# Optimization experiments

Hardware: AMD Instinct MI355X
Metric: run time of the kernel (lower is better)

Reference implementation:

```python
import jax, jax.numpy as jnp
import numpy as np

SIGMA = 0.5          # kernel length_scale
SOFTNESS = 1.0       # softmax temperature scaling
B, F, J, M, U = 4096, 512, 16, 64, 512  # batch, feature, num_domains, domain_dim, units


def _gauss(sqdist):
    # ExponentiatedQuadratic with amplitude=1: exp(-||x-y||^2 / (2*sigma^2))
    return jnp.exp(-sqdist / (2.0 * SIGMA * SIGMA))


def setup_inputs() -> dict:
    key = jax.random.key(0)
    k1, k2, k3 = jax.random.split(key, 3)
    h = jax.random.normal(k1, (B, F), dtype=jnp.float32)
    # domain basis: keras RandomNormal() default stddev=0.05
    domains = 0.05 * jax.random.normal(k2, (J, M, F), dtype=jnp.float32)
    # W_domains: GlorotUniform over (M, U)
    limit = np.sqrt(6.0 / (M + U)).astype(np.float32)
    W = jax.random.uniform(k3, (J, M, U), dtype=jnp.float32, minval=-limit, maxval=limit)
    b = jnp.zeros((J, U), dtype=jnp.float32)
    return {"h": h, "domains": domains, "W": W, "b": b}


def reference(h, domains, W, b):
    # ---- kernel matrix between inputs and all domain bases: K[b,j,m] ----
    h2 = jnp.sum(h * h, axis=-1)                      # [B]
    d2 = jnp.sum(domains * domains, axis=-1)          # [J,M]
    cross = jnp.einsum('bf,jmf->bjm', h, domains)     # [B,J,M]
    K_hd = _gauss(h2[:, None, None] + d2[None] - 2.0 * cross)

    # ---- per-domain MMD: k(x,x) - 2*mean_m k(x,d_m) + mean_{m,m'} k(d_m,d_m') ----
    dd = d2[:, :, None] + d2[:, None, :] - 2.0 * jnp.einsum('jmf,jnf->jmn', domains, domains)
    k_dd_mean = jnp.mean(_gauss(dd), axis=(1, 2))     # [J]
    mmd = 1.0 - 2.0 * jnp.mean(K_hd, axis=2) + k_dd_mean[None, :]  # [B,J]

    # softmax over domains of -softness * mmd  -> domain probabilities [B,J]
    prob = jax.nn.softmax(-SOFTNESS * mmd, axis=1)

    # ---- representer outputs per domain: K(h, D_j) @ W_j + b_j ----
    out = jnp.einsum('bjm,jmu->bju', K_hd, W) + b[None]  # [B,J,U]

    # probability-weighted sum over domains
    return jnp.einsum('bj,bju->bu', prob, out)           # [B,U]
```

## Files before the change

### kernel.cpp

```cpp
#include <hip/hip_runtime.h>
#include <math.h>

typedef unsigned short ushort_t;
typedef __attribute__((ext_vector_type(8))) short bf16x8;
typedef __attribute__((ext_vector_type(4))) float f32x4;

#define B_SZ 4096
#define F_SZ 512
#define J_SZ 16
#define M_SZ 64
#define U_SZ 512
#define P_SZ 1024

__device__ __forceinline__ ushort_t f2bf(float f) {
    union { float f; unsigned int u; } v; v.f = f;
    unsigned int r = (v.u + 0x7FFFu + ((v.u >> 16) & 1u)) >> 16;
    return (ushort_t)r;
}

__device__ __forceinline__ void gload_lds16(const void* g, void* l) {
    __builtin_amdgcn_global_load_lds(
        (const __attribute__((address_space(1))) unsigned int*)g,
        (__attribute__((address_space(3))) unsigned int*)l, 16, 0, 0);
}

__global__ __launch_bounds__(256) void prep_kernel(const float* __restrict__ h,
                                                   const float* __restrict__ dom,
                                                   const float* __restrict__ W,
                                                   ushort_t* __restrict__ hbf,
                                                   ushort_t* __restrict__ dombf,
                                                   ushort_t* __restrict__ Wt,
                                                   float* __restrict__ h2,
                                                   float* __restrict__ d2,
                                                   float* __restrict__ Gpart) {
    const int bid = blockIdx.x;
    const int tid = threadIdx.x;

    if (bid < 1024) {
        int b = bid * 4 + (tid >> 6);
        int lane = tid & 63;
        const float4* row = (const float4*)(h + (size_t)b * F_SZ);
        ushort4* orow = (ushort4*)(hbf + (size_t)b * F_SZ);
        float s = 0.f;
        for (int i = lane; i < F_SZ / 4; i += 64) {
            float4 v = row[i];
            s += v.x * v.x + v.y * v.y + v.z * v.z + v.w * v.w;
            ushort4 o; o.x = f2bf(v.x); o.y = f2bf(v.y); o.z = f2bf(v.z); o.w = f2bf(v.w);
            orow[i] = o;
        }
        for (int off = 32; off; off >>= 1) s += __shfl_down(s, off);
        if (lane == 0) h2[b] = s;
    } else if (bid < 1280) {
        int p = (bid - 1024) * 4 + (tid >> 6);
        int lane = tid & 63;
        const float4* row = (const float4*)(dom + (size_t)p * F_SZ);
        ushort4* orow = (ushort4*)(dombf + (size_t)p * F_SZ);
        float s = 0.f;
        for (int i = lane; i < F_SZ / 4; i += 64) {
            float4 v = row[i];
            s += v.x * v.x + v.y * v.y + v.z * v.z + v.w * v.w;
            ushort4 o; o.x = f2bf(v.x); o.y = f2bf(v.y); o.z = f2bf(v.z); o.w = f2bf(v.w);
            orow[i] = o;
        }
        for (int off = 32; off; off >>= 1) s += __shfl_down(s, off);
        if (lane == 0) d2[p] = s;
    } else if (bid < 1344) {
        int idx = bid - 1280;
        int j = idx >> 2, kc = idx & 3;
        const float* base = dom + (size_t)j * M_SZ * F_SZ + kc * 128;
        __shared__ float As[32][68];
        int tx = tid & 15, ty = tid >> 4;
        float c[4][4] = {};
        for (int kk = 0; kk < 128; kk += 32) {
            for (int l = 0; l < 2; ++l) {
                int s = tid + l * 256;
                int r = s >> 3, c4 = (s & 7) << 2;
                float4 v = *(const float4*)&base[(size_t)r * F_SZ + kk + c4];
                As[c4 + 0][r] = v.x; As[c4 + 1][r] = v.y;
                As[c4 + 2][r] = v.z; As[c4 + 3][r] = v.w;
            }
            __syncthreads();
            for (int k = 0; k < 32; ++k) {
                float a[4], bv[4];
                for (int i = 0; i < 4; ++i) a[i] = As[k][ty * 4 + i];
                for (int i = 0; i < 4; ++i) bv[i] = As[k][tx * 4 + i];
                for (int i = 0; i < 4; ++i)
                    for (int l2 = 0; l2 < 4; ++l2) c[i][l2] += a[i] * bv[l2];
            }
            __syncthreads();
        }
        float* gout = Gpart + ((size_t)kc * 16 + j) * 4096;
        for (int i = 0; i < 4; ++i)
            for (int l2 = 0; l2 < 4; ++l2)
                gout[(ty * 4 + i) * 64 + tx * 4 + l2] = c[i][l2];
    } else {
        int idx = bid - 1344;
        int pt = (idx >> 3) * 64, ut = (idx & 7) * 64;
        __shared__ ushort_t T[64][72];
        for (int l = 0; l < 4; ++l) {
            int s = l * 256 + tid;
            int r = s >> 4, c4 = (s & 15) << 2;
            float4 v = *(const float4*)&W[(size_t)(pt + r) * U_SZ + ut + c4];
            T[c4 + 0][r] = f2bf(v.x); T[c4 + 1][r] = f2bf(v.y);
            T[c4 + 2][r] = f2bf(v.z); T[c4 + 3][r] = f2bf(v.w);
        }
        __syncthreads();
        for (int l = 0; l < 4; ++l) {
            int s = l * 256 + tid;
            int r2 = s >> 4, c4 = (s & 15) << 2;
            ushort4 o; o.x = T[r2][c4 + 0]; o.y = T[r2][c4 + 1];
            o.z = T[r2][c4 + 2]; o.w = T[r2][c4 + 3];
            *(ushort4*)&Wt[(size_t)(ut + r2) * P_SZ + pt + c4] = o;
        }
    }
}

__global__ __launch_bounds__(256) void gemm1_mfma(const ushort_t* __restrict__ hbf,
                                                  const ushort_t* __restrict__ dombf,
                                                  const float* __restrict__ h2,
                                                  const float* __restrict__ d2,
                                                  const float* __restrict__ Gpart,
                                                  ushort_t* __restrict__ Kbf,
                                                  float* __restrict__ sj,
                                                  float* __restrict__ kdd) {
    __shared__ ushort_t smem[24576];
    short* As = (short*)smem;
    short* Bs = (short*)(smem + 8192);
    const int b0 = blockIdx.x * 64;
    const int p0 = blockIdx.y * 128;
    const int tid = threadIdx.x;
    const int wid = tid >> 6, lane = tid & 63;
    const int wm = wid >> 1, wn = wid & 1;
    const int lcol = lane & 15, quad = lane >> 4;

    f32x4 acc[2][4];
    for (int i = 0; i < 2; ++i)
        for (int n = 0; n < 4; ++n) acc[i][n] = (f32x4){0.f, 0.f, 0.f, 0.f};

    for (int kk = 0; kk < F_SZ; kk += 128) {
#pragma unroll
        for (int l = 0; l < 4; ++l) {
            int s = l * 256 + tid;
            int row = s >> 4, c = s & 15;
            int gc = c ^ (row & 15);
            gload_lds16(hbf + (size_t)(b0 + row) * F_SZ + kk + gc * 8, &As[s * 8]);
        }
#pragma unroll
        for (int l = 0; l < 8; ++l) {
            int s = l * 256 + tid;
            int row = s >> 4, c = s & 15;
            int gc = c ^ (row & 15);
            gload_lds16(dombf + (size_t)(p0 + row) * F_SZ + kk + gc * 8, &Bs[s * 8]);
        }
        __syncthreads();
        bf16x8 ar[2][4], br[4][4];
#pragma unroll
        for (int i = 0; i < 2; ++i) {
            int r = wm * 32 + i * 16 + lcol;
#pragma unroll
            for (int ks = 0; ks < 4; ++ks)
                ar[i][ks] = *(const bf16x8*)&As[r * 128 + ((ks * 4 + quad) ^ (r & 15)) * 8];
        }
#pragma unroll
        for (int n = 0; n < 4; ++n) {
            int r = wn * 64 + n * 16 + lcol;
#pragma unroll
            for (int ks = 0; ks < 4; ++ks)
                br[n][ks] = *(const bf16x8*)&Bs[r * 128 + ((ks * 4 + quad) ^ (r & 15)) * 8];
        }
#pragma unroll
        for (int ks = 0; ks < 4; ++ks)
#pragma unroll
            for (int i = 0; i < 2; ++i)
#pragma unroll
                for (int n = 0; n < 4; ++n)
                    acc[i][n] = __builtin_amdgcn_mfma_f32_16x16x32_bf16(ar[i][ks], br[n][ks], acc[i][n], 0, 0, 0);
        __syncthreads();
    }

    const int jg = (p0 >> 6) + wn;
    float d2v[4];
#pragma unroll
    for (int n = 0; n < 4; ++n) d2v[n] = d2[p0 + wn * 64 + n * 16 + lcol];

    unsigned int stash[2][4][2];
#pragma unroll
    for (int i = 0; i < 2; ++i) {
#pragma unroll
        for (int r = 0; r < 4; ++r) {
            int b = b0 + wm * 32 + i * 16 + quad * 4 + r;
            float h2v = h2[b];
            float rs = 0.f;
            ushort_t kv[4];
#pragma unroll
            for (int n = 0; n < 4; ++n) {
                float sq = h2v + d2v[n] - 2.f * acc[i][n][r];
                float kvf = __expf(-2.f * sq);
                kv[n] = f2bf(kvf);
                rs += kvf;
            }
            stash[i][r][0] = (unsigned int)kv[0] | ((unsigned int)kv[1] << 16);
            stash[i][r][1] = (unsigned int)kv[2] | ((unsigned int)kv[3] << 16);
            rs += __shfl_xor(rs, 1);
            rs += __shfl_xor(rs, 2);
            rs += __shfl_xor(rs, 4);
            rs += __shfl_xor(rs, 8);
            if (lcol == 0) sj[(size_t)b * J_SZ + jg] = rs * (1.f / M_SZ);
        }
    }

    ushort_t* LDSC = smem;
#pragma unroll
    for (int i = 0; i < 2; ++i) {
#pragma unroll
        for (int r = 0; r < 4; ++r) {
            int row = wm * 32 + i * 16 + quad * 4 + r;
#pragma unroll
            for (int n = 0; n < 4; ++n) {
                ushort_t v = (ushort_t)(stash[i][r][n >> 1] >> ((n & 1) * 16));
                LDSC[row * 132 + wn * 64 + n * 16 + lcol] = v;
            }
        }
    }
    __syncthreads();
#pragma unroll
    for (int l = 0; l < 8; ++l) {
        int u = l * 256 + tid;
        int row = u >> 5, segc = (u & 31) * 4;
        ushort4 v = *(const ushort4*)&LDSC[row * 132 + segc];
        *(ushort4*)&Kbf[(size_t)(b0 + row) * P_SZ + p0 + segc] = v;
    }

    if (blockIdx.x < 2) {
        __syncthreads();
        float* sd2 = (float*)smem;
        float* red = ((float*)smem) + 64;
        int j = blockIdx.y * 2 + blockIdx.x;
        if (tid < 64) sd2[tid] = d2[j * 64 + tid];
        __syncthreads();
        const float* g0 = Gpart + (size_t)(0 * 16 + j) * 4096;
        const float* g1 = Gpart + (size_t)(1 * 16 + j) * 4096;
        const float* g2 = Gpart + (size_t)(2 * 16 + j) * 4096;
        const float* g3 = Gpart + (size_t)(3 * 16 + j) * 4096;
        float a2 = 0.f;
        for (int s = tid; s < 4096; s += 256) {
            float G = g0[s] + g1[s] + g2[s] + g3[s];
            a2 += __expf(-2.f * (sd2[s >> 6] + sd2[s & 63] - 2.f * G));
        }
        red[tid] = a2;
        __syncthreads();
        for (int off = 128; off; off >>= 1) {
            if (tid < off) red[tid] += red[tid + off];
            __syncthreads();
        }
        if (tid == 0) kdd[j] = red[0] * (1.f / 4096.f);
    }
}

__global__ __launch_bounds__(256) void gemm2_mfma(const ushort_t* __restrict__ Ks,
                                                  const ushort_t* __restrict__ Wt,
                                                  const float* __restrict__ sj,
                                                  const float* __restrict__ kdd,
                                                  const float* __restrict__ bias,
                                                  float* __restrict__ out) {
    __shared__ short As[64 * 128];
    __shared__ short Bs[64 * 128];
    __shared__ float probS[64 * 17];
    __shared__ float biasS[16 * 64];
    __shared__ float kddS[J_SZ];
    const int b0 = blockIdx.x * 64;
    const int u0 = blockIdx.y * 64;
    const int tid = threadIdx.x;
    const int wid = tid >> 6, lane = tid & 63;
    const int wm = wid >> 1, wn = wid & 1;
    const int lcol = lane & 15, quad = lane >> 4;

    if (tid < J_SZ) kddS[tid] = kdd[tid];
    {
        int rowj = tid >> 4, c4 = (tid & 15) << 2;
        *(float4*)&biasS[rowj * 64 + c4] = *(const float4*)&bias[(size_t)rowj * U_SZ + u0 + c4];
    }
    __syncthreads();
    if (tid < 64) {
        int b = b0 + tid;
        float lg[J_SZ], mx = -1e30f;
#pragma unroll
        for (int j = 0; j < J_SZ; ++j) {
            lg[j] = 2.f * sj[(size_t)b * J_SZ + j] - kddS[j] - 1.f;
            mx = fmaxf(mx, lg[j]);
        }
        float ssum = 0.f;
#pragma unroll
        for (int j = 0; j < J_SZ; ++j) { lg[j] = __expf(lg[j] - mx); ssum += lg[j]; }
        float inv = 1.f / ssum;
#pragma unroll
        for (int j = 0; j < J_SZ; ++j) probS[tid * 17 + j] = lg[j] * inv;
    }
    __syncthreads();

    f32x4 acc_tot[2][2];
    for (int i = 0; i < 2; ++i)
        for (int n = 0; n < 2; ++n) acc_tot[i][n] = (f32x4){0.f, 0.f, 0.f, 0.f};

    for (int jb = 0; jb < 8; ++jb) {
        int kk = jb * 128;
#pragma unroll
        for (int l = 0; l < 4; ++l) {
            int s = l * 256 + tid;
            int row = s >> 4, c = s & 15;
            int gc = c ^ (row & 15);
            gload_lds16(Ks + (size_t)(b0 + row) * P_SZ + kk + gc * 8, &As[s * 8]);
            gload_lds16(Wt + (size_t)(u0 + row) * P_SZ + kk + gc * 8, &Bs[s * 8]);
        }
        __syncthreads();
        bf16x8 ar[2][4], br[2][4];
#pragma unroll
        for (int i = 0; i < 2; ++i) {
            int r = wm * 32 + i * 16 + lcol;
#pragma unroll
            for (int ks = 0; ks < 4; ++ks)
                ar[i][ks] = *(const bf16x8*)&As[r * 128 + ((ks * 4 + quad) ^ (r & 15)) * 8];
        }
#pragma unroll
        for (int n = 0; n < 2; ++n) {
            int r = wn * 32 + n * 16 + lcol;
#pragma unroll
            for (int ks = 0; ks < 4; ++ks)
                br[n][ks] = *(const bf16x8*)&Bs[r * 128 + ((ks * 4 + quad) ^ (r & 15)) * 8];
        }
        f32x4 ac0[2][2], ac1[2][2];
#pragma unroll
        for (int i = 0; i < 2; ++i)
#pragma unroll
            for (int n = 0; n < 2; ++n) {
                ac0[i][n] = (f32x4){0.f, 0.f, 0.f, 0.f};
                ac1[i][n] = (f32x4){0.f, 0.f, 0.f, 0.f};
            }
#pragma unroll
        for (int ks = 0; ks < 2; ++ks)
#pragma unroll
            for (int i = 0; i < 2; ++i)
#pragma unroll
                for (int n = 0; n < 2; ++n)
                    ac0[i][n] = __builtin_amdgcn_mfma_f32_16x16x32_bf16(ar[i][ks], br[n][ks], ac0[i][n], 0, 0, 0);
#pragma unroll
        for (int ks = 2; ks < 4; ++ks)
#pragma unroll
            for (int i = 0; i < 2; ++i)
#pragma unroll
                for (int n = 0; n < 2; ++n)
                    ac1[i][n] = __builtin_amdgcn_mfma_f32_16x16x32_bf16(ar[i][ks], br[n][ks], ac1[i][n], 0, 0, 0);
        __syncthreads();
#pragma unroll
        for (int i = 0; i < 2; ++i) {
#pragma unroll
            for (int r = 0; r < 4; ++r) {
                int row = wm * 32 + i * 16 + quad * 4 + r;
                float pf0 = probS[row * 17 + 2 * jb];
                float pf1 = probS[row * 17 + 2 * jb + 1];
#pragma unroll
                for (int n = 0; n < 2; ++n)
                    acc_tot[i][n][r] += pf0 * ac0[i][n][r] + pf1 * ac1[i][n][r];
            }
        }
    }

    float bv[2][J_SZ];
#pragma unroll
    for (int n = 0; n < 2; ++n) {
        int col = wn * 32 + n * 16 + lcol;
#pragma unroll
        for (int j = 0; j < J_SZ; ++j) bv[n][j] = biasS[j * 64 + col];
    }
#pragma unroll
    for (int i = 0; i < 2; ++i) {
#pragma unroll
        for (int r = 0; r < 4; ++r) {
            int row = wm * 32 + i * 16 + quad * 4 + r;
            int b = b0 + row;
#pragma unroll
            for (int n = 0; n < 2; ++n) {
                float a = acc_tot[i][n][r];
#pragma unroll
                for (int j = 0; j < J_SZ; ++j) a += probS[row * 17 + j] * bv[n][j];
                out[(size_t)b * U_SZ + u0 + wn * 32 + n * 16 + lcol] = a;
            }
        }
    }
}

extern "C" void kernel_launch(void* const* d_in, const int* in_sizes, int n_in,
                              void* d_out, int out_size, void* d_ws, size_t ws_size,
                              hipStream_t stream) {
    const float* h    = (const float*)d_in[0];
    const float* dom  = (const float*)d_in[1];
    const float* W    = (const float*)d_in[2];
    const float* bias = (const float*)d_in[3];
    float* out = (float*)d_out;

    char* ws = (char*)d_ws;
    ushort_t* hbf   = (ushort_t*)ws;  ws += (size_t)B_SZ * F_SZ * 2;
    ushort_t* dombf = (ushort_t*)ws;  ws += (size_t)P_SZ * F_SZ * 2;
    ushort_t* Wt    = (ushort_t*)ws;  ws += (size_t)U_SZ * P_SZ * 2;
    ushort_t* Kbf   = (ushort_t*)ws;  ws += (size_t)B_SZ * P_SZ * 2;
    float* h2    = (float*)ws;  ws += B_SZ * 4;
    float* d2    = (float*)ws;  ws += P_SZ * 4;
    float* kdd   = (float*)ws;  ws += 64;
    float* sj    = (float*)ws;  ws += (size_t)B_SZ * J_SZ * 4;
    float* Gpart = (float*)ws;  ws += (size_t)4 * J_SZ * M_SZ * M_SZ * 4;

    prep_kernel<<<1472, 256, 0, stream>>>(h, dom, W, hbf, dombf, Wt, h2, d2, Gpart);
    gemm1_mfma<<<dim3(B_SZ / 64, P_SZ / 128), 256, 0, stream>>>(hbf, dombf, h2, d2, Gpart, Kbf, sj, kdd);
    gemm2_mfma<<<dim3(B_SZ / 64, U_SZ / 64), 256, 0, stream>>>(Kbf, Wt, sj, kdd, bias, out);
}
```

Before: 103.6 us.

## Compute domain Gram term with MFMA blocks inside gemm1 instead of FP32 prep

Drops the FP32 scalar Gram-matrix path from the prep kernel and the Gpart workspace. Instead, two extra column blocks per grid row in gemm1 multiply the bf16 domain bases against themselves on the MFMA path and reduce exp(-2*sqdist) directly into kdd. This removes 64 prep blocks and the Gpart write/read round trip. In exchange, kdd is now computed from bf16 inputs rather than FP32, and the grid grows from 64 to 66 blocks in x.

```diff
diff --git a/kernel.cpp b/kernel.cpp
--- a/kernel.cpp
+++ b/kernel.cpp
@@ -31,8 +31,7 @@
                                                    ushort_t* __restrict__ dombf,
                                                    ushort_t* __restrict__ Wt,
                                                    float* __restrict__ h2,
-                                                   float* __restrict__ d2,
-                                                   float* __restrict__ Gpart) {
+                                                   float* __restrict__ d2) {
     const int bid = blockIdx.x;
     const int tid = threadIdx.x;
 
@@ -64,37 +63,8 @@
         }
         for (int off = 32; off; off >>= 1) s += __shfl_down(s, off);
         if (lane == 0) d2[p] = s;
-    } else if (bid < 1344) {
+    } else {
         int idx = bid - 1280;
-        int j = idx >> 2, kc = idx & 3;
-        const float* base = dom + (size_t)j * M_SZ * F_SZ + kc * 128;
-        __shared__ float As[32][68];
-        int tx = tid & 15, ty = tid >> 4;
-        float c[4][4] = {};
-        for (int kk = 0; kk < 128; kk += 32) {
-            for (int l = 0; l < 2; ++l) {
-                int s = tid + l * 256;
-                int r = s >> 3, c4 = (s & 7) << 2;
-                float4 v = *(const float4*)&base[(size_t)r * F_SZ + kk + c4];
-                As[c4 + 0][r] = v.x; As[c4 + 1][r] = v.y;
-                As[c4 + 2][r] = v.z; As[c4 + 3][r] = v.w;
-            }
-            __syncthreads();
-            for (int k = 0; k < 32; ++k) {
-                float a[4], bv[4];
-                for (int i = 0; i < 4; ++i) a[i] = As[k][ty * 4 + i];
-                for (int i = 0; i < 4; ++i) bv[i] = As[k][tx * 4 + i];
-                for (int i = 0; i < 4; ++i)
-                    for (int l2 = 0; l2 < 4; ++l2) c[i][l2] += a[i] * bv[l2];
-            }
-            __syncthreads();
-        }
-        float* gout = Gpart + ((size_t)kc * 16 + j) * 4096;
-        for (int i = 0; i < 4; ++i)
-            for (int l2 = 0; l2 < 4; ++l2)
-                gout[(ty * 4 + i) * 64 + tx * 4 + l2] = c[i][l2];
-    } else {
-        int idx = bid - 1344;
         int pt = (idx >> 3) * 64, ut = (idx & 7) * 64;
         __shared__ ushort_t T[64][72];
         for (int l = 0; l < 4; ++l) {
@@ -119,15 +89,17 @@
                                                   const ushort_t* __restrict__ dombf,
                                                   const float* __restrict__ h2,
                                                   const float* __restrict__ d2,
-                                                  const float* __restrict__ Gpart,
                                                   ushort_t* __restrict__ Kbf,
                                                   float* __restrict__ sj,
                                                   float* __restrict__ kdd) {
     __shared__ ushort_t smem[24576];
     short* As = (short*)smem;
     short* Bs = (short*)(smem + 8192);
-    const int b0 = blockIdx.x * 64;
+    const int xb = blockIdx.x;
     const int p0 = blockIdx.y * 128;
+    const bool gramBlk = (xb < 2);
+    const int b0 = gramBlk ? (p0 + xb * 64) : (xb - 2) * 64;
+    const ushort_t* Aglob = gramBlk ? dombf : hbf;
     const int tid = threadIdx.x;
     const int wid = tid >> 6, lane = tid & 63;
     const int wm = wid >> 1, wn = wid & 1;
@@ -143,7 +115,7 @@
             int s = l * 256 + tid;
             int row = s >> 4, c = s & 15;
             int gc = c ^ (row & 15);
-            gload_lds16(hbf + (size_t)(b0 + row) * F_SZ + kk + gc * 8, &As[s * 8]);
+            gload_lds16(Aglob + (size_t)(b0 + row) * F_SZ + kk + gc * 8, &As[s * 8]);
         }
 #pragma unroll
         for (int l = 0; l < 8; ++l) {
@@ -178,11 +150,39 @@
         __syncthreads();
     }
 
+    float d2v[4];
+#pragma unroll
+    for (int n = 0; n < 4; ++n) d2v[n] = d2[p0 + wn * 64 + n * 16 + lcol];
+
+    if (gramBlk) {
+        int j = blockIdx.y * 2 + xb;
+        float s = 0.f;
+        if (wn == xb) {
+#pragma unroll
+            for (int i = 0; i < 2; ++i) {
+#pragma unroll
+                for (int r = 0; r < 4; ++r) {
+                    float d2r = d2[b0 + wm * 32 + i * 16 + quad * 4 + r];
+#pragma unroll
+                    for (int n = 0; n < 4; ++n) {
+                        float sq = d2r + d2v[n] - 2.f * acc[i][n][r];
+                        s += __expf(-2.f * sq);
+                    }
+                }
+            }
+        }
+        float* red = (float*)smem;
+        red[tid] = s;
+        __syncthreads();
+        for (int off = 128; off; off >>= 1) {
+            if (tid < off) red[tid] += red[tid + off];
+            __syncthreads();
+        }
+        if (tid == 0) kdd[j] = red[0] * (1.f / 4096.f);
+        return;
+    }
+
     const int jg = (p0 >> 6) + wn;
-    float d2v[4];
-#pragma unroll
-    for (int n = 0; n < 4; ++n) d2v[n] = d2[p0 + wn * 64 + n * 16 + lcol];
-
     unsigned int stash[2][4][2];
 #pragma unroll
     for (int i = 0; i < 2; ++i) {
@@ -229,31 +229,6 @@
         int row = u >> 5, segc = (u & 31) * 4;
         ushort4 v = *(const ushort4*)&LDSC[row * 132 + segc];
         *(ushort4*)&Kbf[(size_t)(b0 + row) * P_SZ + p0 + segc] = v;
-    }
-
-    if (blockIdx.x < 2) {
-        __syncthreads();
-        float* sd2 = (float*)smem;
-        float* red = ((float*)smem) + 64;
-        int j = blockIdx.y * 2 + blockIdx.x;
-        if (tid < 64) sd2[tid] = d2[j * 64 + tid];
-        __syncthreads();
-        const float* g0 = Gpart + (size_t)(0 * 16 + j) * 4096;
-        const float* g1 = Gpart + (size_t)(1 * 16 + j) * 4096;
-        const float* g2 = Gpart + (size_t)(2 * 16 + j) * 4096;
-        const float* g3 = Gpart + (size_t)(3 * 16 + j) * 4096;
-        float a2 = 0.f;
-        for (int s = tid; s < 4096; s += 256) {
-            float G = g0[s] + g1[s] + g2[s] + g3[s];
-            a2 += __expf(-2.f * (sd2[s >> 6] + sd2[s & 63] - 2.f * G));
-        }
-        red[tid] = a2;
-        __syncthreads();
-        for (int off = 128; off; off >>= 1) {
-            if (tid < off) red[tid] += red[tid + off];
-            __syncthreads();
-        }
-        if (tid == 0) kdd[j] = red[0] * (1.f / 4096.f);
     }
 }
 
@@ -403,13 +378,12 @@
     ushort_t* dombf = (ushort_t*)ws;  ws += (size_t)P_SZ * F_SZ * 2;
     ushort_t* Wt    = (ushort_t*)ws;  ws += (size_t)U_SZ * P_SZ * 2;
     ushort_t* Kbf   = (ushort_t*)ws;  ws += (size_t)B_SZ * P_SZ * 2;
-    float* h2    = (float*)ws;  ws += B_SZ * 4;
-    float* d2    = (float*)ws;  ws += P_SZ * 4;
-    float* kdd   = (float*)ws;  ws += 64;
-    float* sj    = (float*)ws;  ws += (size_t)B_SZ * J_SZ * 4;
-    float* Gpart = (float*)ws;  ws += (size_t)4 * J_SZ * M_SZ * M_SZ * 4;
-
-    prep_kernel<<<1472, 256, 0, stream>>>(h, dom, W, hbf, dombf, Wt, h2, d2, Gpart);
-    gemm1_mfma<<<dim3(B_SZ / 64, P_SZ / 128), 256, 0, stream>>>(hbf, dombf, h2, d2, Gpart, Kbf, sj, kdd);
+    float* h2  = (float*)ws;  ws += B_SZ * 4;
+    float* d2  = (float*)ws;  ws += P_SZ * 4;
+    float* kdd = (float*)ws;  ws += 64;
+    float* sj  = (float*)ws;  ws += (size_t)B_SZ * J_SZ * 4;
+
+    prep_kernel<<<1408, 256, 0, stream>>>(h, dom, W, hbf, dombf, Wt, h2, d2);
+    gemm1_mfma<<<dim3(66, P_SZ / 128), 256, 0, stream>>>(hbf, dombf, h2, d2, Kbf, sj, kdd);
     gemm2_mfma<<<dim3(B_SZ / 64, U_SZ / 64), 256, 0, stream>>>(Kbf, Wt, sj, kdd, bias, out);
 }
```

Measured after the change: 95.16 us. -8.2%, faster.
